# Performance work log

Measured on AMD Instinct MI355X. Metric: run time of the kernel, lower is better.

The kernel has to match this reference:

```python
import jax, jax.numpy as jnp
import numpy as np

ALPHA = 1.5
N_ITER = 50
B, N, C = 8, 1024, 1024
H = 8
D = C // H


def entmax_bisect(x, alpha=ALPHA, n_iter=N_ITER):
    # entmax-bisect (Peters et al. 2019), matching the entmax package's bisection.
    xm = (alpha - 1.0) * x
    d = xm.shape[-1]
    inv = 1.0 / (alpha - 1.0)  # = 2.0 for alpha=1.5
    max_val = jnp.max(xm, axis=-1, keepdims=True)
    tau_lo = max_val - 1.0                                   # gp(1, alpha) = 1
    tau_hi = max_val - (1.0 / d) ** (alpha - 1.0)            # gp(1/d, alpha)
    f_lo = jnp.sum(jnp.maximum(xm - tau_lo, 0.0) ** inv, axis=-1, keepdims=True) - 1.0
    dm0 = tau_hi - tau_lo

    def body(_, carry):
        tau_lo, dm, tau_m = carry
        dm = dm * 0.5
        tau_m = tau_lo + dm
        f_m = jnp.sum(jnp.maximum(xm - tau_m, 0.0) ** inv, axis=-1, keepdims=True) - 1.0
        tau_lo = jnp.where(f_m * f_lo >= 0, tau_m, tau_lo)
        return (tau_lo, dm, tau_m)

    _, _, tau_m = jax.lax.fori_loop(0, n_iter, body, (tau_lo, dm0, tau_lo))
    p = jnp.maximum(xm - tau_m, 0.0) ** inv
    return p / jnp.sum(p, axis=-1, keepdims=True)


def setup_inputs() -> dict:
    key = jax.random.key(0)
    ks = jax.random.split(key, 9)
    s = 0.02
    return {
        "x": jax.random.normal(ks[0], (B, N, C), dtype=jnp.float32),
        "Wq": jax.random.normal(ks[1], (C, C), dtype=jnp.float32) * s,
        "bq": jnp.zeros((C,), dtype=jnp.float32),
        "Wk": jax.random.normal(ks[2], (C, C), dtype=jnp.float32) * s,
        "bk": jnp.zeros((C,), dtype=jnp.float32),
        "Wv": jax.random.normal(ks[3], (C, C), dtype=jnp.float32) * s,
        "bv": jnp.zeros((C,), dtype=jnp.float32),
        "Wo": jax.random.normal(ks[4], (C, C), dtype=jnp.float32) * s,
        "bo": jnp.zeros((C,), dtype=jnp.float32),
    }


def reference(x, Wq, bq, Wk, bk, Wv, bv, Wo, bo):
    b, n, c = x.shape
    def proj(W, bias):
        return (x @ W + bias).reshape(b, n, H, D).transpose(0, 2, 1, 3)  # [B,H,N,D]
    q = proj(Wq, bq)
    k = proj(Wk, bk)
    v = proj(Wv, bv)
    scores = jnp.einsum("bhnd,bhmd->bhnm", q, k) / (D ** 0.5)  # [B,H,N,N]
    attn = entmax_bisect(scores)
    ctx = jnp.einsum("bhnm,bhmd->bhnd", attn, v)
    ctx = ctx.transpose(0, 2, 1, 3).reshape(b, n, c)
    out = ctx @ Wo + bo
    return (out, attn)
```

## Files before the change

kernel.cpp:

```cpp
#include <hip/hip_runtime.h>

#define DEV __device__ __forceinline__

typedef _Float16 f16;
typedef _Float16 f16x8 __attribute__((ext_vector_type(8)));
typedef float f32x4 __attribute__((ext_vector_type(4)));


DEV void gload_lds16(const f16* g, f16* l) {
  __builtin_amdgcn_global_load_lds(
      (const __attribute__((address_space(1))) void*)g,
      (__attribute__((address_space(3))) void*)l, 16, 0, 0);
}

DEV float wred_max(float v) {
#pragma unroll
  for (int o = 32; o > 0; o >>= 1) v = fmaxf(v, __shfl_xor(v, o, 64));
  return v;
}
DEV float wred_sum(float v) {
#pragma unroll
  for (int o = 32; o > 0; o >>= 1) v += __shfl_xor(v, o, 64);
  return v;
}


__global__ __launch_bounds__(256) void cast_f32_f16(const float* __restrict__ in,
                                                    f16* __restrict__ out, int n) {
  int i = (blockIdx.x * 256 + threadIdx.x) * 4;
  if (i < n) {
    float4 f = *(const float4*)(in + i);
    f16 o0 = (f16)f.x, o1 = (f16)f.y, o2 = (f16)f.z, o3 = (f16)f.w;
    f16* d = out + i;
    d[0] = o0; d[1] = o1; d[2] = o2; d[3] = o3;
  }
}

__global__ __launch_bounds__(256) void transpose_cast(
    const float* s0, const float* s1, const float* s2, const float* s3,
    f16* d0, f16* d1, f16* d2, f16* d3) {
  const float* S[4] = {s0, s1, s2, s3};
  f16* D[4] = {d0, d1, d2, d3};
  const float* W = S[blockIdx.z];
  f16* WT = D[blockIdx.z];
  __shared__ float tile[32][33];
  int tx = threadIdx.x, ty = threadIdx.y;
  int r0 = blockIdx.y * 32, c0 = blockIdx.x * 32;
#pragma unroll
  for (int i = 0; i < 32; i += 8) tile[ty + i][tx] = W[(r0 + ty + i) * 1024 + c0 + tx];
  __syncthreads();
#pragma unroll
  for (int i = 0; i < 32; i += 8) WT[(c0 + ty + i) * 1024 + r0 + tx] = (f16)tile[tx][ty + i];
}


DEV void gemm_bt_f16(const f16* __restrict__ A, const f16* __restrict__ B,
                     int lda, int ldb, int K, f16* As, f16* Bs, f32x4 (&acc)[4][4]) {
  const int t = threadIdx.x;
  const int l = t & 63, w = t >> 6;
  const int wm = w >> 1, wn = w & 1;
  const f16* ag = A + (t >> 2) * lda + (t & 3) * 8;
  const f16* bg = B + (t >> 2) * ldb + (t & 3) * 8;
  f16* asd = As + w * 512;
  f16* bsd = Bs + w * 512;
  const int arow = wm * 64 + (l & 15);
  const int brow = wn * 64 + (l & 15);
  const int ko = (l >> 4) * 8;
  for (int k0 = 0; k0 < K; k0 += 32) {
    __syncthreads();
    gload_lds16(ag + k0, asd);
    gload_lds16(ag + 64 * lda + k0, asd + 2048);
    gload_lds16(bg + k0, bsd);
    gload_lds16(bg + 64 * ldb + k0, bsd + 2048);
    __syncthreads();
    f16x8 af[4], bf[4];
#pragma unroll
    for (int i = 0; i < 4; i++) af[i] = *(const f16x8*)(As + (arow + i * 16) * 32 + ko);
#pragma unroll
    for (int j = 0; j < 4; j++) bf[j] = *(const f16x8*)(Bs + (brow + j * 16) * 32 + ko);
#pragma unroll
    for (int i = 0; i < 4; i++)
#pragma unroll
      for (int j = 0; j < 4; j++)
        acc[i][j] = __builtin_amdgcn_mfma_f32_16x16x32_f16(af[i], bf[j], acc[i][j], 0, 0, 0);
  }
}


__global__ __launch_bounds__(256) void qkv_gemm(
    const f16* __restrict__ xb, const f16* __restrict__ WTq, const f16* __restrict__ WTk,
    const f16* __restrict__ WTv, const float* __restrict__ bq, const float* __restrict__ bk,
    const float* __restrict__ bv, f16* __restrict__ q, f16* __restrict__ kk,
    f16* __restrict__ vT) {
  __shared__ f16 As[128 * 32];
  __shared__ f16 Bs[128 * 32];
  __shared__ f16 tr[128 * 132];
  const int z = blockIdx.z;
  const f16* WT = (z == 0) ? WTq : ((z == 1) ? WTk : WTv);
  const float* bias = (z == 0) ? bq : ((z == 1) ? bk : bv);
  const int rowBase = blockIdx.y * 128, colBase = blockIdx.x * 128;
  f32x4 zero4 = {0.f, 0.f, 0.f, 0.f};
  f32x4 acc[4][4];
#pragma unroll
  for (int i = 0; i < 4; i++)
#pragma unroll
    for (int j = 0; j < 4; j++) acc[i][j] = zero4;
  gemm_bt_f16(xb + rowBase * 1024, WT + colBase * 1024, 1024, 1024, 1024, As, Bs, acc);
  const int t = threadIdx.x, l = t & 63, w = t >> 6, wm = w >> 1, wn = w & 1;
  if (z < 2) {
    f16* dst = (z == 0) ? q : kk;
#pragma unroll
    for (int i = 0; i < 4; i++)
#pragma unroll
      for (int j = 0; j < 4; j++)
#pragma unroll
        for (int r = 0; r < 4; r++) {
          int rt = wm * 64 + i * 16 + ((l >> 4) << 2) + r;
          int ct = wn * 64 + j * 16 + (l & 15);
          int rr = rowBase + rt, c = colBase + ct;
          float val = acc[i][j][r] + bias[c];
          int b = rr >> 10, n = rr & 1023, h = c >> 7, d = c & 127;
          dst[((b * 8 + h) * 1024 + n) * 128 + d] = (f16)val;
        }
  } else {
#pragma unroll
    for (int i = 0; i < 4; i++)
#pragma unroll
      for (int j = 0; j < 4; j++)
#pragma unroll
        for (int r = 0; r < 4; r++) {
          int rt = wm * 64 + i * 16 + ((l >> 4) << 2) + r;
          int ct = wn * 64 + j * 16 + (l & 15);
          tr[ct * 132 + rt] = (f16)(acc[i][j][r] + bias[colBase + ct]);
        }
    __syncthreads();
    int b = blockIdx.y >> 3, h = blockIdx.x;
    int nb = (blockIdx.y & 7) * 128;
    int head = b * 8 + h;
#pragma unroll
    for (int p = 0; p < 8; p++) {
      int lin = p * 2048 + t * 8;
      int c = lin >> 7, r = lin & 127;
      const f16* src = &tr[c * 132 + r];
      uint2 a0 = *(const uint2*)(src);
      uint2 a1 = *(const uint2*)(src + 4);
      f16* dst = vT + head * 131072 + c * 1024 + nb + r;
      *(uint2*)(dst) = a0;
      *(uint2*)(dst + 4) = a1;
    }
  }
}


__global__ __launch_bounds__(256) void scores_gemm(const f16* __restrict__ q,
                                                   const f16* __restrict__ kk,
                                                   f16* __restrict__ xm16) {
  __shared__ f16 As[128 * 32];
  __shared__ f16 Bs[128 * 32];
  const int head = blockIdx.z;
  const int rowBase = blockIdx.y * 128, colBase = blockIdx.x * 128;
  f32x4 zero4 = {0.f, 0.f, 0.f, 0.f};
  f32x4 acc[4][4];
#pragma unroll
  for (int i = 0; i < 4; i++)
#pragma unroll
    for (int j = 0; j < 4; j++) acc[i][j] = zero4;
  gemm_bt_f16(q + head * 131072 + rowBase * 128, kk + head * 131072 + colBase * 128,
              128, 128, 128, As, Bs, acc);
  const float SC = 0.04419417382415922f;
  const int l = threadIdx.x & 63, w = threadIdx.x >> 6, wm = w >> 1, wn = w & 1;
  f16* out = xm16 + (size_t)head * 1048576;
#pragma unroll
  for (int i = 0; i < 4; i++)
#pragma unroll
    for (int j = 0; j < 4; j++)
#pragma unroll
      for (int r = 0; r < 4; r++) {
        int rt = wm * 64 + i * 16 + ((l >> 4) << 2) + r;
        int ct = wn * 64 + j * 16 + (l & 15);
        out[(size_t)(rowBase + rt) * 1024 + colBase + ct] = (f16)(acc[i][j][r] * SC);
      }
}


__global__ __launch_bounds__(512) void entmax_rows(f16* __restrict__ xm16,
                                                   float* __restrict__ attn) {
  const int l = threadIdx.x & 63, w = threadIdx.x >> 6;
  const size_t row = (size_t)blockIdx.x * 8 + w;
  f16* xp = xm16 + row * 1024;
  float* ap = attn + row * 1024;
  f16x8 h0 = *(const f16x8*)(xp + l * 8);
  f16x8 h1 = *(const f16x8*)(xp + 512 + l * 8);
  float xr[16];
#pragma unroll
  for (int e = 0; e < 8; e++) { xr[e] = (float)h0[e]; xr[8 + e] = (float)h1[e]; }
  float mx = xr[0];
#pragma unroll
  for (int e = 1; e < 16; e++) mx = fmaxf(mx, xr[e]);
  mx = wred_max(mx);
  float tau_lo = mx - 1.0f;
  float tau_hi = mx - 0.03125f;
  float dm = tau_hi - tau_lo;
  float s = 0.f;
#pragma unroll
  for (int e = 0; e < 16; e++) { float tv = fmaxf(xr[e] - tau_lo, 0.f); s = fmaf(tv, tv, s); }
  s = wred_sum(s);
  const float f_lo = s - 1.0f;
  float tau_m = tau_lo;
  for (int it = 0; it < 16; ++it) {
    dm *= 0.5f;
    tau_m = tau_lo + dm;
    float sm = 0.f;
#pragma unroll
    for (int e = 0; e < 16; e++) { float tv = fmaxf(xr[e] - tau_m, 0.f); sm = fmaf(tv, tv, sm); }
    sm = wred_sum(sm);
    if ((sm - 1.0f) * f_lo >= 0.f) tau_lo = tau_m;
  }
  float p[16];
  float ps = 0.f;
#pragma unroll
  for (int e = 0; e < 16; e++) { float tv = fmaxf(xr[e] - tau_m, 0.f); p[e] = tv * tv; ps += p[e]; }
  ps = wred_sum(ps);
  float inv = 1.0f / ps;
  float4 v0 = {p[0] * inv, p[1] * inv, p[2] * inv, p[3] * inv};
  float4 v1 = {p[4] * inv, p[5] * inv, p[6] * inv, p[7] * inv};
  float4 v2 = {p[8] * inv, p[9] * inv, p[10] * inv, p[11] * inv};
  float4 v3 = {p[12] * inv, p[13] * inv, p[14] * inv, p[15] * inv};
  *(float4*)(ap + l * 8) = v0;
  *(float4*)(ap + l * 8 + 4) = v1;
  *(float4*)(ap + 512 + l * 8) = v2;
  *(float4*)(ap + 512 + l * 8 + 4) = v3;
  f16x8 o0 = {(f16)v0.x, (f16)v0.y, (f16)v0.z, (f16)v0.w,
              (f16)v1.x, (f16)v1.y, (f16)v1.z, (f16)v1.w};
  f16x8 o1 = {(f16)v2.x, (f16)v2.y, (f16)v2.z, (f16)v2.w,
              (f16)v3.x, (f16)v3.y, (f16)v3.z, (f16)v3.w};
  *(f16x8*)(xp + l * 8) = o0;
  *(f16x8*)(xp + 512 + l * 8) = o1;
}


__global__ __launch_bounds__(256) void ctx_gemm(const f16* __restrict__ p16,
                                                const f16* __restrict__ vT,
                                                f16* __restrict__ ctx) {
  __shared__ f16 As[128 * 32];
  __shared__ f16 Bs[128 * 32];
  const int head = blockIdx.z;
  const int rowBase = blockIdx.y * 128;
  f32x4 zero4 = {0.f, 0.f, 0.f, 0.f};
  f32x4 acc[4][4];
#pragma unroll
  for (int i = 0; i < 4; i++)
#pragma unroll
    for (int j = 0; j < 4; j++) acc[i][j] = zero4;
  gemm_bt_f16(p16 + (size_t)head * 1048576 + (size_t)rowBase * 1024,
              vT + head * 131072, 1024, 1024, 1024, As, Bs, acc);
  const int l = threadIdx.x & 63, w = threadIdx.x >> 6, wm = w >> 1, wn = w & 1;
  int b = head >> 3, h = head & 7;
#pragma unroll
  for (int i = 0; i < 4; i++)
#pragma unroll
    for (int j = 0; j < 4; j++)
#pragma unroll
      for (int r = 0; r < 4; r++) {
        int rt = wm * 64 + i * 16 + ((l >> 4) << 2) + r;
        int ct = wn * 64 + j * 16 + (l & 15);
        int n = rowBase + rt;
        ctx[(size_t)(b * 1024 + n) * 1024 + h * 128 + ct] = (f16)acc[i][j][r];
      }
}


__global__ __launch_bounds__(256) void out_gemm(const f16* __restrict__ ctx,
                                                const f16* __restrict__ WTo,
                                                const float* __restrict__ bo,
                                                float* __restrict__ out) {
  __shared__ f16 As[128 * 32];
  __shared__ f16 Bs[128 * 32];
  const int rowBase = blockIdx.y * 128, colBase = blockIdx.x * 128;
  f32x4 zero4 = {0.f, 0.f, 0.f, 0.f};
  f32x4 acc[4][4];
#pragma unroll
  for (int i = 0; i < 4; i++)
#pragma unroll
    for (int j = 0; j < 4; j++) acc[i][j] = zero4;
  gemm_bt_f16(ctx + rowBase * 1024, WTo + colBase * 1024, 1024, 1024, 1024, As, Bs, acc);
  const int l = threadIdx.x & 63, w = threadIdx.x >> 6, wm = w >> 1, wn = w & 1;
#pragma unroll
  for (int i = 0; i < 4; i++)
#pragma unroll
    for (int j = 0; j < 4; j++)
#pragma unroll
      for (int r = 0; r < 4; r++) {
        int rt = wm * 64 + i * 16 + ((l >> 4) << 2) + r;
        int ct = wn * 64 + j * 16 + (l & 15);
        out[(size_t)(rowBase + rt) * 1024 + colBase + ct] = acc[i][j][r] + bo[colBase + ct];
      }
}


extern "C" void kernel_launch(void* const* d_in, const int* in_sizes, int n_in,
                              void* d_out, int out_size, void* d_ws, size_t ws_size,
                              hipStream_t stream) {
  const float* x  = (const float*)d_in[0];
  const float* Wq = (const float*)d_in[1];
  const float* bq = (const float*)d_in[2];
  const float* Wk = (const float*)d_in[3];
  const float* bk = (const float*)d_in[4];
  const float* Wv = (const float*)d_in[5];
  const float* bv = (const float*)d_in[6];
  const float* Wo = (const float*)d_in[7];
  const float* bo = (const float*)d_in[8];
  float* out = (float*)d_out;
  float* attn = out + 8388608;

  char* ws = (char*)d_ws;
  f16* xb  = (f16*)(ws);
  f16* ctx = (f16*)(ws);
  f16* WTq = (f16*)(ws + (16u << 20));
  f16* WTk = (f16*)(ws + (18u << 20));
  f16* WTv = (f16*)(ws + (20u << 20));
  f16* WTo = (f16*)(ws + (22u << 20));
  f16* q   = (f16*)(ws + (24u << 20));
  f16* kk  = (f16*)(ws + (40u << 20));
  f16* vT  = (f16*)(ws + (56u << 20));
  f16* xm16= (f16*)(ws + (72u << 20));

  cast_f32_f16<<<dim3(8192), dim3(256), 0, stream>>>(x, xb, 8388608);
  transpose_cast<<<dim3(32, 32, 4), dim3(32, 8), 0, stream>>>(
      Wq, Wk, Wv, Wo, WTq, WTk, WTv, WTo);
  qkv_gemm<<<dim3(8, 64, 3), dim3(256), 0, stream>>>(
      xb, WTq, WTk, WTv, bq, bk, bv, q, kk, vT);
  scores_gemm<<<dim3(8, 8, 64), dim3(256), 0, stream>>>(q, kk, xm16);
  entmax_rows<<<dim3(8192), dim3(512), 0, stream>>>(xm16, attn);
  ctx_gemm<<<dim3(1, 8, 64), dim3(256), 0, stream>>>(xm16, vT, ctx);
  out_gemm<<<dim3(8, 64), dim3(256), 0, stream>>>(ctx, WTo, bo, out);
}
```

Baseline: 604.6 us.

## Fuse scores GEMM, entmax bisection and context GEMM into one attention kernel

Replaces three separate kernels with one kernel that handles 16 query rows per block. Each block computes the scores against all 1024 keys into LDS, runs the entmax bisection on two rows per wave, writes the fp32 attention output, and then multiplies the fp16 probabilities by V straight from LDS. This avoids the fp16 score matrix round trip through global memory and two kernel launches. In exchange each block reloads all of K and V for just 16 rows, so K/V traffic rises and MFMA utilisation per block is low.

```diff
diff --git a/kernel.cpp b/kernel.cpp
--- a/kernel.cpp
+++ b/kernel.cpp
@@ -11,17 +11,6 @@
   __builtin_amdgcn_global_load_lds(
       (const __attribute__((address_space(1))) void*)g,
       (__attribute__((address_space(3))) void*)l, 16, 0, 0);
-}
-
-DEV float wred_max(float v) {
-#pragma unroll
-  for (int o = 32; o > 0; o >>= 1) v = fmaxf(v, __shfl_xor(v, o, 64));
-  return v;
-}
-DEV float wred_sum(float v) {
-#pragma unroll
-  for (int o = 32; o > 0; o >>= 1) v += __shfl_xor(v, o, 64);
-  return v;
 }
 
 
@@ -152,121 +141,143 @@
 }
 
 
-__global__ __launch_bounds__(256) void scores_gemm(const f16* __restrict__ q,
-                                                   const f16* __restrict__ kk,
-                                                   f16* __restrict__ xm16) {
-  __shared__ f16 As[128 * 32];
-  __shared__ f16 Bs[128 * 32];
-  const int head = blockIdx.z;
-  const int rowBase = blockIdx.y * 128, colBase = blockIdx.x * 128;
-  f32x4 zero4 = {0.f, 0.f, 0.f, 0.f};
-  f32x4 acc[4][4];
-#pragma unroll
-  for (int i = 0; i < 4; i++)
-#pragma unroll
-    for (int j = 0; j < 4; j++) acc[i][j] = zero4;
-  gemm_bt_f16(q + head * 131072 + rowBase * 128, kk + head * 131072 + colBase * 128,
-              128, 128, 128, As, Bs, acc);
+#define PSLD 1032
+
+__global__ __launch_bounds__(512, 4) void fused_attn(
+    const f16* __restrict__ q, const f16* __restrict__ kk,
+    const f16* __restrict__ vT, float* __restrict__ attn, f16* __restrict__ ctx) {
+  __shared__ f16 Ps[16 * PSLD];
+  __shared__ f16 Ks[128 * 128];
+  const int t = threadIdx.x, l = t & 63, w = t >> 6;
+  const int head = blockIdx.y, n0 = blockIdx.x * 16;
+  const int l15 = l & 15, l16 = l >> 4;
+
+  const f16* qh = q + head * 131072 + n0 * 128;
+  f16x8 qf[4];
+#pragma unroll
+  for (int it = 0; it < 4; it++)
+    qf[it] = *(const f16x8*)(qh + l15 * 128 + it * 32 + l16 * 8);
+
   const float SC = 0.04419417382415922f;
-  const int l = threadIdx.x & 63, w = threadIdx.x >> 6, wm = w >> 1, wn = w & 1;
-  f16* out = xm16 + (size_t)head * 1048576;
-#pragma unroll
-  for (int i = 0; i < 4; i++)
-#pragma unroll
-    for (int j = 0; j < 4; j++)
-#pragma unroll
-      for (int r = 0; r < 4; r++) {
-        int rt = wm * 64 + i * 16 + ((l >> 4) << 2) + r;
-        int ct = wn * 64 + j * 16 + (l & 15);
-        out[(size_t)(rowBase + rt) * 1024 + colBase + ct] = (f16)(acc[i][j][r] * SC);
+  const f16* kh = kk + head * 131072;
+  for (int cb = 0; cb < 8; cb++) {
+    __syncthreads();
+#pragma unroll
+    for (int c2 = 0; c2 < 4; c2++) {
+      int n = c2 * 32 + (t >> 4);
+      int ch = (t & 15) ^ (n & 15);
+      gload_lds16(kh + (cb * 128 + n) * 128 + ch * 8, Ks + c2 * 4096 + w * 512);
+    }
+    __syncthreads();
+    const int nrow = w * 16 + l15;
+    f32x4 acc = {0.f, 0.f, 0.f, 0.f};
+#pragma unroll
+    for (int it = 0; it < 4; it++) {
+      int g = it * 4 + l16;
+      f16x8 bf = *(const f16x8*)(Ks + nrow * 128 + ((g ^ (nrow & 15)) * 8));
+      acc = __builtin_amdgcn_mfma_f32_16x16x32_f16(qf[it], bf, acc, 0, 0, 0);
+    }
+    const int n = cb * 128 + nrow;
+#pragma unroll
+    for (int r = 0; r < 4; r++) {
+      int m = l16 * 4 + r;
+      Ps[m * PSLD + n] = (f16)(acc[r] * SC);
+    }
+  }
+
+  __syncthreads();
+  {
+    f16* r0p = Ps + (w * 2) * PSLD;
+    f16* r1p = r0p + PSLD;
+    float x0[16], x1[16];
+#pragma unroll
+    for (int j = 0; j < 16; j++) {
+      x0[j] = (float)r0p[j * 64 + l];
+      x1[j] = (float)r1p[j * 64 + l];
+    }
+    float m0 = x0[0], m1 = x1[0];
+#pragma unroll
+    for (int j = 1; j < 16; j++) { m0 = fmaxf(m0, x0[j]); m1 = fmaxf(m1, x1[j]); }
+#pragma unroll
+    for (int o = 32; o; o >>= 1) {
+      m0 = fmaxf(m0, __shfl_xor(m0, o, 64));
+      m1 = fmaxf(m1, __shfl_xor(m1, o, 64));
+    }
+    float lo0 = m0 - 1.0f, lo1 = m1 - 1.0f;
+    float s0 = 0.f, s1 = 0.f;
+#pragma unroll
+    for (int j = 0; j < 16; j++) {
+      float a = fmaxf(x0[j] - lo0, 0.f); s0 = fmaf(a, a, s0);
+      float b = fmaxf(x1[j] - lo1, 0.f); s1 = fmaf(b, b, s1);
+    }
+#pragma unroll
+    for (int o = 32; o; o >>= 1) { s0 += __shfl_xor(s0, o, 64); s1 += __shfl_xor(s1, o, 64); }
+    const float fl0 = s0 - 1.0f, fl1 = s1 - 1.0f;
+    float dm = 0.96875f;
+    float tm0 = lo0, tm1 = lo1;
+    for (int it = 0; it < 16; ++it) {
+      dm *= 0.5f;
+      tm0 = lo0 + dm; tm1 = lo1 + dm;
+      float a0 = 0.f, a1 = 0.f;
+#pragma unroll
+      for (int j = 0; j < 16; j++) {
+        float a = fmaxf(x0[j] - tm0, 0.f); a0 = fmaf(a, a, a0);
+        float b = fmaxf(x1[j] - tm1, 0.f); a1 = fmaf(b, b, a1);
       }
-}
-
-
-__global__ __launch_bounds__(512) void entmax_rows(f16* __restrict__ xm16,
-                                                   float* __restrict__ attn) {
-  const int l = threadIdx.x & 63, w = threadIdx.x >> 6;
-  const size_t row = (size_t)blockIdx.x * 8 + w;
-  f16* xp = xm16 + row * 1024;
-  float* ap = attn + row * 1024;
-  f16x8 h0 = *(const f16x8*)(xp + l * 8);
-  f16x8 h1 = *(const f16x8*)(xp + 512 + l * 8);
-  float xr[16];
-#pragma unroll
-  for (int e = 0; e < 8; e++) { xr[e] = (float)h0[e]; xr[8 + e] = (float)h1[e]; }
-  float mx = xr[0];
-#pragma unroll
-  for (int e = 1; e < 16; e++) mx = fmaxf(mx, xr[e]);
-  mx = wred_max(mx);
-  float tau_lo = mx - 1.0f;
-  float tau_hi = mx - 0.03125f;
-  float dm = tau_hi - tau_lo;
-  float s = 0.f;
-#pragma unroll
-  for (int e = 0; e < 16; e++) { float tv = fmaxf(xr[e] - tau_lo, 0.f); s = fmaf(tv, tv, s); }
-  s = wred_sum(s);
-  const float f_lo = s - 1.0f;
-  float tau_m = tau_lo;
-  for (int it = 0; it < 16; ++it) {
-    dm *= 0.5f;
-    tau_m = tau_lo + dm;
-    float sm = 0.f;
-#pragma unroll
-    for (int e = 0; e < 16; e++) { float tv = fmaxf(xr[e] - tau_m, 0.f); sm = fmaf(tv, tv, sm); }
-    sm = wred_sum(sm);
-    if ((sm - 1.0f) * f_lo >= 0.f) tau_lo = tau_m;
-  }
-  float p[16];
-  float ps = 0.f;
-#pragma unroll
-  for (int e = 0; e < 16; e++) { float tv = fmaxf(xr[e] - tau_m, 0.f); p[e] = tv * tv; ps += p[e]; }
-  ps = wred_sum(ps);
-  float inv = 1.0f / ps;
-  float4 v0 = {p[0] * inv, p[1] * inv, p[2] * inv, p[3] * inv};
-  float4 v1 = {p[4] * inv, p[5] * inv, p[6] * inv, p[7] * inv};
-  float4 v2 = {p[8] * inv, p[9] * inv, p[10] * inv, p[11] * inv};
-  float4 v3 = {p[12] * inv, p[13] * inv, p[14] * inv, p[15] * inv};
-  *(float4*)(ap + l * 8) = v0;
-  *(float4*)(ap + l * 8 + 4) = v1;
-  *(float4*)(ap + 512 + l * 8) = v2;
-  *(float4*)(ap + 512 + l * 8 + 4) = v3;
-  f16x8 o0 = {(f16)v0.x, (f16)v0.y, (f16)v0.z, (f16)v0.w,
-              (f16)v1.x, (f16)v1.y, (f16)v1.z, (f16)v1.w};
-  f16x8 o1 = {(f16)v2.x, (f16)v2.y, (f16)v2.z, (f16)v2.w,
-              (f16)v3.x, (f16)v3.y, (f16)v3.z, (f16)v3.w};
-  *(f16x8*)(xp + l * 8) = o0;
-  *(f16x8*)(xp + 512 + l * 8) = o1;
-}
-
-
-__global__ __launch_bounds__(256) void ctx_gemm(const f16* __restrict__ p16,
-                                                const f16* __restrict__ vT,
-                                                f16* __restrict__ ctx) {
-  __shared__ f16 As[128 * 32];
-  __shared__ f16 Bs[128 * 32];
-  const int head = blockIdx.z;
-  const int rowBase = blockIdx.y * 128;
-  f32x4 zero4 = {0.f, 0.f, 0.f, 0.f};
-  f32x4 acc[4][4];
-#pragma unroll
-  for (int i = 0; i < 4; i++)
-#pragma unroll
-    for (int j = 0; j < 4; j++) acc[i][j] = zero4;
-  gemm_bt_f16(p16 + (size_t)head * 1048576 + (size_t)rowBase * 1024,
-              vT + head * 131072, 1024, 1024, 1024, As, Bs, acc);
-  const int l = threadIdx.x & 63, w = threadIdx.x >> 6, wm = w >> 1, wn = w & 1;
-  int b = head >> 3, h = head & 7;
-#pragma unroll
-  for (int i = 0; i < 4; i++)
-#pragma unroll
-    for (int j = 0; j < 4; j++)
-#pragma unroll
-      for (int r = 0; r < 4; r++) {
-        int rt = wm * 64 + i * 16 + ((l >> 4) << 2) + r;
-        int ct = wn * 64 + j * 16 + (l & 15);
-        int n = rowBase + rt;
-        ctx[(size_t)(b * 1024 + n) * 1024 + h * 128 + ct] = (f16)acc[i][j][r];
-      }
+#pragma unroll
+      for (int o = 32; o; o >>= 1) { a0 += __shfl_xor(a0, o, 64); a1 += __shfl_xor(a1, o, 64); }
+      if ((a0 - 1.0f) * fl0 >= 0.f) lo0 = tm0;
+      if ((a1 - 1.0f) * fl1 >= 0.f) lo1 = tm1;
+    }
+    float q0 = 0.f, q1 = 0.f;
+#pragma unroll
+    for (int j = 0; j < 16; j++) {
+      float a = fmaxf(x0[j] - tm0, 0.f); x0[j] = a * a; q0 += x0[j];
+      float b = fmaxf(x1[j] - tm1, 0.f); x1[j] = b * b; q1 += x1[j];
+    }
+#pragma unroll
+    for (int o = 32; o; o >>= 1) { q0 += __shfl_xor(q0, o, 64); q1 += __shfl_xor(q1, o, 64); }
+    float i0 = 1.0f / q0, i1 = 1.0f / q1;
+    float* a0p = attn + ((size_t)head * 1024 + n0 + w * 2) * 1024;
+    float* a1p = a0p + 1024;
+#pragma unroll
+    for (int j = 0; j < 16; j++) {
+      float v0 = x0[j] * i0, v1 = x1[j] * i1;
+      a0p[j * 64 + l] = v0;
+      a1p[j * 64 + l] = v1;
+      r0p[j * 64 + l] = (f16)v0;
+      r1p[j * 64 + l] = (f16)v1;
+    }
+  }
+
+  const f16* vh = vT + head * 131072;
+  f16* Vs = Ks;
+  f32x4 cacc = {0.f, 0.f, 0.f, 0.f};
+  for (int k0 = 0; k0 < 1024; k0 += 64) {
+    __syncthreads();
+#pragma unroll
+    for (int c2 = 0; c2 < 2; c2++) {
+      int d = c2 * 64 + (t >> 3);
+      int ch = (t & 7) ^ (d & 7);
+      gload_lds16(vh + d * 1024 + k0 + ch * 8, Vs + c2 * 4096 + w * 512);
+    }
+    __syncthreads();
+    const int drow = w * 16 + l15;
+#pragma unroll
+    for (int kb = 0; kb < 2; kb++) {
+      f16x8 af = *(const f16x8*)(Ps + l15 * PSLD + k0 + kb * 32 + l16 * 8);
+      int g = kb * 4 + l16;
+      f16x8 bf = *(const f16x8*)(Vs + drow * 64 + ((g ^ (drow & 7)) * 8));
+      cacc = __builtin_amdgcn_mfma_f32_16x16x32_f16(af, bf, cacc, 0, 0, 0);
+    }
+  }
+  const int b = head >> 3, h = head & 7;
+#pragma unroll
+  for (int r = 0; r < 4; r++) {
+    int m = l16 * 4 + r;
+    int d = w * 16 + l15;
+    ctx[(size_t)(b * 1024 + n0 + m) * 1024 + h * 128 + d] = (f16)cacc[r];
+  }
 }
 
 
@@ -323,15 +334,12 @@
   f16* q   = (f16*)(ws + (24u << 20));
   f16* kk  = (f16*)(ws + (40u << 20));
   f16* vT  = (f16*)(ws + (56u << 20));
-  f16* xm16= (f16*)(ws + (72u << 20));
 
   cast_f32_f16<<<dim3(8192), dim3(256), 0, stream>>>(x, xb, 8388608);
   transpose_cast<<<dim3(32, 32, 4), dim3(32, 8), 0, stream>>>(
       Wq, Wk, Wv, Wo, WTq, WTk, WTv, WTo);
   qkv_gemm<<<dim3(8, 64, 3), dim3(256), 0, stream>>>(
       xb, WTq, WTk, WTv, bq, bk, bv, q, kk, vT);
-  scores_gemm<<<dim3(8, 8, 64), dim3(256), 0, stream>>>(q, kk, xm16);
-  entmax_rows<<<dim3(8192), dim3(512), 0, stream>>>(xm16, attn);
-  ctx_gemm<<<dim3(1, 8, 64), dim3(256), 0, stream>>>(xm16, vT, ctx);
+  fused_attn<<<dim3(64, 64), dim3(512), 0, stream>>>(q, kk, vT, attn, ctx);
   out_gemm<<<dim3(8, 64), dim3(256), 0, stream>>>(ctx, WTo, bo, out);
 }
```

New measurement: 667.0 us. +10.3%, slower.
